# Performance work log

Measured on AMD Instinct MI355X. Metric: run time of the kernel, lower is better.

The kernel has to match this reference:

```python
import jax, jax.numpy as jnp
import numpy as np

N_NODES = 100_000
N_EDGES = 1_600_000
IN_C, HID_C, OUT_C = 128, 64, 32


def gcn_conv(x, W, b, src, dst, n_nodes):
    """PyG GCNConv with add_self_loops=True, symmetric normalization.
    out = D^{-1/2} (A + I) D^{-1/2} (x @ W) + b, with D = deg(A) + 1.
    Self-loop contribution added analytically to avoid materializing loop edges."""
    h = x @ W                                            # [N, F_out]
    deg = jnp.zeros((n_nodes,), h.dtype).at[dst].add(1.0) + 1.0
    dinv = jax.lax.rsqrt(deg)                            # deg >= 1 from self-loops
    norm = dinv[src] * dinv[dst]                         # [E]
    agg = jnp.zeros_like(h).at[dst].add(h[src] * norm[:, None])
    agg = agg + h * (dinv * dinv)[:, None]               # self-loop term
    return agg + b


def setup_inputs() -> dict:
    key = jax.random.key(0)
    ks = jax.random.split(key, 9)
    x = jax.random.normal(ks[0], (N_NODES, IN_C), dtype=jnp.float32)
    edge_index = jax.random.randint(ks[1], (2, N_EDGES), 0, N_NODES, dtype=jnp.int64)
    g = lambda k, fi, fo: jax.random.normal(k, (fi, fo), jnp.float32) * np.sqrt(2.0 / (fi + fo)).astype(np.float32)
    W1 = g(ks[2], IN_C, HID_C)
    b1 = jnp.zeros((HID_C,), jnp.float32)
    W2 = g(ks[3], HID_C, OUT_C)
    b2 = jnp.zeros((OUT_C,), jnp.float32)
    Wl = g(ks[4], IN_C + HID_C + OUT_C, OUT_C)
    bl = jnp.zeros((OUT_C,), jnp.float32)
    return {"x": x, "edge_index": edge_index, "W1": W1, "b1": b1,
            "W2": W2, "b2": b2, "Wl": Wl, "bl": bl}


def reference(x, edge_index, W1, b1, W2, b2, Wl, bl):
    src, dst = edge_index[0], edge_index[1]
    n = x.shape[0]
    h1 = jax.nn.relu(gcn_conv(x, W1, b1, src, dst, n))   # dropout is identity in eval
    h2 = gcn_conv(h1, W2, b2, src, dst, n)
    cat = jnp.concatenate([x, h1, h2], axis=1)           # [N, in+hid+out]
    return jax.nn.log_softmax(cat @ Wl + bl, axis=-1)
```

## Files before the change

### kernel.cpp

```cpp
#include <hip/hip_runtime.h>
#include <hip/hip_bf16.h>
#include <hip/hip_fp16.h>

typedef __hip_bfloat16 bf16;
typedef __attribute__((ext_vector_type(8))) short short8;
typedef __attribute__((ext_vector_type(4))) float f32x4;
typedef __attribute__((ext_vector_type(2))) float f32x2;
typedef _Float16 h16x2 __attribute__((ext_vector_type(2)));

#define MFMA16(a, b, c) __builtin_amdgcn_mfma_f32_16x16x32_bf16((a), (b), (c), 0, 0, 0)

static __device__ __forceinline__ float ldf(const void* p, long long i, bool f32) {
    return f32 ? ((const float*)p)[i] : __bfloat162float(((const bf16*)p)[i]);
}

static __device__ __forceinline__ short f2bs(float v) {
    union { bf16 h; short s; } u; u.h = __float2bfloat16(v); return u.s;
}

static __device__ __forceinline__ unsigned int pack_bf16x2(float a, float b) {
    return (unsigned int)(unsigned short)f2bs(a) | ((unsigned int)(unsigned short)f2bs(b) << 16);
}

static __device__ __forceinline__ unsigned int pack_h2(float a, float b) {
    __half2 hh = __floats2half2_rn(a, b);
    union { __half2 h; unsigned int u; } cv; cv.h = hh; return cv.u;
}

static __device__ __forceinline__ h16x2 as_h2(unsigned int u) {
    union { unsigned int u; h16x2 h; } cv; cv.u = u; return cv.h;
}

static __device__ __forceinline__ unsigned char f32_to_fp8(float v) {
    int pk = __builtin_amdgcn_cvt_pk_fp8_f32(v, 0.f, 0, false);
    return (unsigned char)(pk & 0xFF);
}
static __device__ __forceinline__ f32x2 fp8x2_to_f32x2(unsigned short v) {
    return __builtin_amdgcn_cvt_pk_f32_fp8((int)v, false);
}

static __device__ __forceinline__ int ld_src(const int* ei, int E, int e, bool i64) {
    return i64 ? ei[2 * e] : ei[e];
}
static __device__ __forceinline__ int ld_dst(const int* ei, int E, int e, bool i64) {
    return i64 ? ei[2 * (E + e)] : ei[E + e];
}


__global__ __launch_bounds__(256, 4)
void bhist_kernel(const int* __restrict__ ei, int E,
                  const void* __restrict__ x, const void* __restrict__ W1,
                  const void* __restrict__ Wl,
                  int shift, int NB, int nchunk,
                  int* __restrict__ flags, int* __restrict__ bucketCount,
                  bf16* __restrict__ Bp1, bf16* __restrict__ Bp3) {
    __shared__ int h[256];
    __shared__ int sdet;
    int bid = blockIdx.x;
    if (bid >= nchunk) {
        int which = bid - nchunk;
        const void* W = which ? Wl : W1;
        bf16* Bp = which ? Bp3 : Bp1;
        int ntiles = which ? 2 : 4, nc = which ? 32 : 64, nfrag = which ? 14 : 16;
        if (threadIdx.x == 0) sdet = 0;
        __syncthreads();
        const unsigned short* u = (const unsigned short*)W;
        int bad = 0;
        for (int i = threadIdx.x; i < 4096; i += 256) {
            unsigned e = (u[i] >> 7) & 0xFF;
            if (e >= 0xA0) bad++;
        }
        if (bad) atomicAdd(&sdet, bad);
        __syncthreads();
        bool fw = sdet > 16;
        if (which == 0 && threadIdx.x == 0) flags[1] = fw ? 1 : 0;
        for (int s = threadIdx.x; s < nfrag * 64; s += 256) {
            int f = s >> 6, lane = s & 63;
            int kstep = f / ntiles, ntile = f % ntiles;
            int n = ntile * 16 + (lane & 15);
            int kbase = kstep * 32 + (lane >> 4) * 8;
#pragma unroll
            for (int j = 0; j < 8; j++)
                Bp[s * 8 + j] = __float2bfloat16(ldf(W, (long long)(kbase + j) * nc + n, fw));
        }
        return;
    }
    if (bid == 0) {
        if (threadIdx.x == 0) sdet = 0;
        __syncthreads();
        const unsigned short* u = (const unsigned short*)x;
        int bad = 0;
        for (int i = threadIdx.x; i < 4096; i += 256) {
            unsigned e = (u[i] >> 7) & 0xFF;
            if (e >= 0xA0) bad++;
        }
        if (bad) atomicAdd(&sdet, bad);
        __syncthreads();
        if (threadIdx.x == 0) flags[0] = (sdet > 16) ? 1 : 0;
        __syncthreads();
    }
    if (threadIdx.x == 0) sdet = 0;
    for (int i = threadIdx.x; i < 256; i += 256) h[i] = 0;
    __syncthreads();
    {
        int nz = 0;
        for (int i = threadIdx.x; i < 1024; i += 256)
            if (2 * i + 1 < 2 * E && ei[2 * i + 1] != 0) nz++;
        if (nz) atomicAdd(&sdet, nz);
    }
    __syncthreads();
    bool i64 = (sdet == 0);
    int base = bid * 4096;
    for (int i = 0; i < 16; i++) {
        int e = base + i * 256 + threadIdx.x;
        if (e < E) atomicAdd(&h[ld_dst(ei, E, e, i64) >> shift], 1);
    }
    __syncthreads();
    for (int i = threadIdx.x; i < NB; i += 256)
        if (h[i]) atomicAdd(&bucketCount[i], h[i]);
}

__global__ __launch_bounds__(256, 4)
void bpart_kernel(const int* __restrict__ ei, int E, int shift, int NB,
                  const int* __restrict__ bucketCount, int* __restrict__ bcursor,
                  int2* __restrict__ ebuf) {
    __shared__ int h[256];
    __shared__ int gofs[256];
    __shared__ int bs[256];
    __shared__ int2 se[4096];
    __shared__ int sdet;
    if (threadIdx.x == 0) sdet = 0;
    for (int i = threadIdx.x; i < 256; i += 256) h[i] = 0;
    __syncthreads();
    {
        int nz = 0;
        for (int i = threadIdx.x; i < 1024; i += 256)
            if (2 * i + 1 < 2 * E && ei[2 * i + 1] != 0) nz++;
        if (nz) atomicAdd(&sdet, nz);
    }
    __syncthreads();
    bool i64 = (sdet == 0);
    int base = blockIdx.x * 4096;
    for (int i = 0; i < 16; i++) {
        int e = base + i * 256 + threadIdx.x;
        if (e < E) {
            int s = ld_src(ei, E, e, i64), d = ld_dst(ei, E, e, i64);
            se[i * 256 + threadIdx.x] = make_int2(s, d);
            atomicAdd(&h[d >> shift], 1);
        }
    }
    int v = ((int)threadIdx.x < NB) ? bucketCount[threadIdx.x] : 0;
    bs[threadIdx.x] = v;
    __syncthreads();
    for (int off = 1; off < 256; off <<= 1) {
        int t = ((int)threadIdx.x >= off) ? bs[threadIdx.x - off] : 0;
        __syncthreads();
        bs[threadIdx.x] += t;
        __syncthreads();
    }
    if ((int)threadIdx.x < NB) {
        int c = h[threadIdx.x];
        int b0 = bs[threadIdx.x] - v;
        gofs[threadIdx.x] = c ? (b0 + atomicAdd(&bcursor[threadIdx.x], c)) : 0;
    }
    __syncthreads();
    for (int i = threadIdx.x; i < 256; i += 256) h[i] = 0;
    __syncthreads();
    for (int i = 0; i < 16; i++) {
        int e = base + i * 256 + threadIdx.x;
        if (e < E) {
            int2 w = se[i * 256 + threadIdx.x];
            int b = w.y >> shift;
            int p = atomicAdd(&h[b], 1);
            ebuf[gofs[b] + p] = w;
        }
    }
}

__global__ __launch_bounds__(256, 2)
void bbuild_kernel(const int2* __restrict__ ebuf, const int* __restrict__ bucketCount,
                   int shift, int N, int E, int* __restrict__ rowptr,
                   float* __restrict__ dinv, int* __restrict__ csr_src) {
    __shared__ int cnt[1024];
    __shared__ int exc[1024];
    __shared__ int bs[256];
    int b = blockIdx.x;
    int v = ((int)threadIdx.x < 256) ? bucketCount[threadIdx.x] : 0;
    bs[threadIdx.x] = v;
    __syncthreads();
    for (int off = 1; off < 256; off <<= 1) {
        int t = ((int)threadIdx.x >= off) ? bs[threadIdx.x - off] : 0;
        __syncthreads();
        bs[threadIdx.x] += t;
        __syncthreads();
    }
    int end = bs[b];
    int beg = end - bucketCount[b];
    __syncthreads();
    int nodeBase = b << shift;
    int width = 1 << shift;
    int nn = N - nodeBase; if (nn > width) nn = width;
    for (int i = threadIdx.x; i < width; i += 256) cnt[i] = 0;
    __syncthreads();
    for (int e = beg + threadIdx.x; e < end; e += 256)
        atomicAdd(&cnt[ebuf[e].y - nodeBase], 1);
    __syncthreads();
    int per = width / 256;
    int s = 0;
    int base4 = threadIdx.x * per;
    for (int i = 0; i < per; i++) s += cnt[base4 + i];
    bs[threadIdx.x] = s;
    __syncthreads();
    for (int off = 1; off < 256; off <<= 1) {
        int t = ((int)threadIdx.x >= off) ? bs[threadIdx.x - off] : 0;
        __syncthreads();
        bs[threadIdx.x] += t;
        __syncthreads();
    }
    int run = bs[threadIdx.x] - s;
    for (int i = 0; i < per; i++) { exc[base4 + i] = run; run += cnt[base4 + i]; }
    __syncthreads();
    for (int i = threadIdx.x; i < nn; i += 256) {
        int node = nodeBase + i;
        rowptr[node] = beg + exc[i];
        dinv[node] = rsqrtf((float)cnt[i] + 1.0f);
    }
    __syncthreads();
    for (int i = threadIdx.x; i < width; i += 256) cnt[i] = 0;
    __syncthreads();
    for (int e = beg + threadIdx.x; e < end; e += 256) {
        int2 w = ebuf[e];
        int l = w.y - nodeBase;
        int p = atomicAdd(&cnt[l], 1);
        csr_src[beg + exc[l] + p] = w.x;
    }
    if (b == 0 && threadIdx.x == 0) rowptr[N] = E;
}

__global__ __launch_bounds__(256, 3)
void gemm1_mfma_kernel(const void* __restrict__ x, const bf16* __restrict__ Bpack,
                       const float* __restrict__ dinv, const int* __restrict__ flags,
                       unsigned char* __restrict__ h1g, short* __restrict__ xb, int N) {
    bool fx = flags[0] != 0;
    int lane = threadIdx.x & 63, wave = threadIdx.x >> 6;
    int m = lane & 15, quad = lane >> 4;
    int base = blockIdx.x * 128 + wave * 32;
    if (base >= N) return;
    const short8* bp = (const short8*)Bpack;
    short8 B[16];
#pragma unroll
    for (int i = 0; i < 16; i++) B[i] = bp[i * 64 + lane];
    if (base + 32 <= N) {
#pragma unroll
        for (int t = 0; t < 2; t++) {
            int r0 = base + t * 16;
            short8 A[4];
            if (fx) {
                const float* xr = &((const float*)x)[(long long)(r0 + m) * 128 + quad * 8];
#pragma unroll
                for (int k = 0; k < 4; k++) {
                    float4 fa = *(const float4*)(xr + k * 32);
                    float4 fb = *(const float4*)(xr + k * 32 + 4);
                    short8 o;
                    o[0] = f2bs(fa.x); o[1] = f2bs(fa.y); o[2] = f2bs(fa.z); o[3] = f2bs(fa.w);
                    o[4] = f2bs(fb.x); o[5] = f2bs(fb.y); o[6] = f2bs(fb.z); o[7] = f2bs(fb.w);
                    A[k] = o;
                }
                short* xw = &xb[(long long)(r0 + m) * 128 + quad * 8];
#pragma unroll
                for (int k = 0; k < 4; k++) *(short8*)(xw + k * 32) = A[k];
            } else {
                const short* xr = &((const short*)x)[(long long)(r0 + m) * 128 + quad * 8];
#pragma unroll
                for (int k = 0; k < 4; k++) A[k] = *(const short8*)(xr + k * 32);
            }
            f32x4 acc[4];
#pragma unroll
            for (int nt = 0; nt < 4; nt++) acc[nt] = (f32x4){0.f, 0.f, 0.f, 0.f};
#pragma unroll
            for (int k = 0; k < 4; k++) {
#pragma unroll
                for (int nt = 0; nt < 4; nt++) acc[nt] = MFMA16(A[k], B[k * 4 + nt], acc[nt]);
            }
            float dv[4];
#pragma unroll
            for (int r = 0; r < 4; r++) dv[r] = dinv[r0 + quad * 4 + r];
            unsigned char* o = &h1g[(long long)(r0 + quad * 4) * 64 + m];
#pragma unroll
            for (int nt = 0; nt < 4; nt++) {
#pragma unroll
                for (int r = 0; r < 4; r++) o[(long long)r * 64 + nt * 16] = f32_to_fp8(acc[nt][r] * dv[r]);
            }
        }
    } else {
#pragma unroll
        for (int t = 0; t < 2; t++) {
            int r0 = base + t * 16;
            int row = r0 + m;
            short8 A[4];
#pragma unroll
            for (int k = 0; k < 4; k++) A[k] = (short8){0,0,0,0,0,0,0,0};
            if (row < N) {
                if (fx) {
                    const float* xr = &((const float*)x)[(long long)row * 128 + quad * 8];
#pragma unroll
                    for (int k = 0; k < 4; k++) {
                        float4 fa = *(const float4*)(xr + k * 32);
                        float4 fb = *(const float4*)(xr + k * 32 + 4);
                        short8 o;
                        o[0] = f2bs(fa.x); o[1] = f2bs(fa.y); o[2] = f2bs(fa.z); o[3] = f2bs(fa.w);
                        o[4] = f2bs(fb.x); o[5] = f2bs(fb.y); o[6] = f2bs(fb.z); o[7] = f2bs(fb.w);
                        A[k] = o;
                    }
                    short* xw = &xb[(long long)row * 128 + quad * 8];
#pragma unroll
                    for (int k = 0; k < 4; k++) *(short8*)(xw + k * 32) = A[k];
                } else {
                    const short* xr = &((const short*)x)[(long long)row * 128 + quad * 8];
#pragma unroll
                    for (int k = 0; k < 4; k++) A[k] = *(const short8*)(xr + k * 32);
                }
            }
            f32x4 acc[4];
#pragma unroll
            for (int nt = 0; nt < 4; nt++) acc[nt] = (f32x4){0.f, 0.f, 0.f, 0.f};
#pragma unroll
            for (int k = 0; k < 4; k++) {
#pragma unroll
                for (int nt = 0; nt < 4; nt++) acc[nt] = MFMA16(A[k], B[k * 4 + nt], acc[nt]);
            }
#pragma unroll
            for (int r = 0; r < 4; r++) {
                int orow = r0 + quad * 4 + r;
                if (orow < N) {
                    float dv = dinv[orow];
                    unsigned char* o = &h1g[(long long)orow * 64 + m];
#pragma unroll
                    for (int nt = 0; nt < 4; nt++) o[nt * 16] = f32_to_fp8(acc[nt][r] * dv);
                }
            }
        }
    }
}

__global__ __launch_bounds__(256, 8)
void gather1_kernel(const unsigned short* __restrict__ h1g, const float* __restrict__ dinv,
                    const int* __restrict__ rowptr, const int* __restrict__ csr_src,
                    const void* __restrict__ bptr, const void* __restrict__ W2,
                    const int* __restrict__ flags,
                    unsigned int* __restrict__ h1b, __half* __restrict__ h2g, int N) {
    __shared__ unsigned int w2p[1024];
    __shared__ unsigned int h1s[4][2][32];
    bool fw = flags[1] != 0;
    for (int j = threadIdx.x; j < 1024; j += 256) {
        int k2 = j >> 5, c0 = j & 31;
        float a = ldf(W2, (long long)(2 * k2) * 32 + c0, fw);
        float b = ldf(W2, (long long)(2 * k2 + 1) * 32 + c0, fw);
        w2p[j] = pack_h2(a, b);
    }
    __syncthreads();
    int lane = threadIdx.x & 63;
    int c = lane & 31, hf = lane >> 5;
    int wv = __builtin_amdgcn_readfirstlane(threadIdx.x >> 6);
    int n0 = (blockIdx.x * 4 + wv) * 2;
    if (n0 >= N) return;
    bool has1 = (n0 + 1 < N);
    int beg = rowptr[n0];
    int mid = rowptr[n0 + 1];
    int end = has1 ? rowptr[n0 + 2] : mid;
    const unsigned short* hL = h1g + c;
    float aA0 = 0.f, aA1 = 0.f;
    float aN0 = 0.f, aN1 = 0.f;
    int p = beg;
    for (; p + 32 <= end; p += 32) {
        unsigned short v[16]; float r[16];
#pragma unroll
        for (int u = 0; u < 16; u++) {
            int s0 = csr_src[p + 2 * u];
            int s1 = csr_src[p + 2 * u + 1];
            int s = hf ? s1 : s0;
            r[u] = ((p + 2 * u + hf) < mid) ? 1.f : 0.f;
            v[u] = hL[(long long)s * 32];
        }
#pragma unroll
        for (int u = 0; u < 16; u++) {
            f32x2 f = fp8x2_to_f32x2(v[u]);
            aA0 += f.x; aA1 += f.y;
            aN0 = fmaf(f.x, r[u], aN0);
            aN1 = fmaf(f.y, r[u], aN1);
        }
    }
    for (; p + 16 <= end; p += 16) {
        unsigned short v[8]; float r[8];
#pragma unroll
        for (int u = 0; u < 8; u++) {
            int s0 = csr_src[p + 2 * u];
            int s1 = csr_src[p + 2 * u + 1];
            int s = hf ? s1 : s0;
            r[u] = ((p + 2 * u + hf) < mid) ? 1.f : 0.f;
            v[u] = hL[(long long)s * 32];
        }
#pragma unroll
        for (int u = 0; u < 8; u++) {
            f32x2 f = fp8x2_to_f32x2(v[u]);
            aA0 += f.x; aA1 += f.y;
            aN0 = fmaf(f.x, r[u], aN0);
            aN1 = fmaf(f.y, r[u], aN1);
        }
    }
    if (p < end) {
        unsigned short v[8]; float mk[8], r[8];
#pragma unroll
        for (int u = 0; u < 8; u++) {
            int i0 = p + 2 * u, i1 = i0 + 1;
            int s0 = csr_src[(i0 < end) ? i0 : beg];
            int s1 = csr_src[(i1 < end) ? i1 : beg];
            int s = hf ? s1 : s0;
            int i = p + 2 * u + hf;
            mk[u] = (i < end) ? 1.f : 0.f;
            r[u]  = (i < mid) ? 1.f : 0.f;
            v[u] = hL[(long long)s * 32];
        }
#pragma unroll
        for (int u = 0; u < 8; u++) {
            f32x2 f = fp8x2_to_f32x2(v[u]);
            aA0 = fmaf(f.x, mk[u], aA0);
            aA1 = fmaf(f.y, mk[u], aA1);
            aN0 = fmaf(f.x, r[u], aN0);
            aN1 = fmaf(f.y, r[u], aN1);
        }
    }
    aA0 += __shfl_xor(aA0, 32); aA1 += __shfl_xor(aA1, 32);
    aN0 += __shfl_xor(aN0, 32); aN1 += __shfl_xor(aN1, 32);
    int node = n0 + hf;
    int nodeC = (node < N) ? node : n0;
    float a0 = hf ? (aA0 - aN0) : aN0;
    float a1 = hf ? (aA1 - aN1) : aN1;
    f32x2 gs = fp8x2_to_f32x2(h1g[(long long)nodeC * 32 + c]);
    float dvd = dinv[nodeC];
    float o0 = fmaxf(dvd * (a0 + gs.x) + ldf(bptr, 2 * c, fw), 0.f);
    float o1 = fmaxf(dvd * (a1 + gs.y) + ldf(bptr, 2 * c + 1, fw), 0.f);
    if (node < N)
        h1b[(long long)node * 32 + c] = pack_bf16x2(o0, o1);
    h1s[wv][hf][c] = pack_h2(o0, o1);
    __threadfence_block();
    const unsigned int* hrow = h1s[wv][hf];
    float acc = 0.f;
#pragma unroll 8
    for (int k2 = 0; k2 < 32; k2++)
        acc = __builtin_amdgcn_fdot2(as_h2(hrow[k2]), as_h2(w2p[k2 * 32 + c]), acc, false);
    if (node < N)
        h2g[(long long)node * 32 + c] = __float2half(dvd * acc);
}

__global__ __launch_bounds__(256, 8)
void gather2_kernel(const unsigned int* __restrict__ h2g, const float* __restrict__ dinv,
                    const int* __restrict__ rowptr, const int* __restrict__ csr_src,
                    const void* __restrict__ bptr, const int* __restrict__ flags,
                    unsigned int* __restrict__ h2b, int N) {
    bool fw = flags[1] != 0;
    int lane = threadIdx.x & 63;
    int c = lane & 15, sub = lane >> 4;
    int wv = __builtin_amdgcn_readfirstlane(threadIdx.x >> 6);
    int n0 = (blockIdx.x * 4 + wv) * 2;
    if (n0 >= N) return;
    bool has1 = (n0 + 1 < N);
    int beg = rowptr[n0];
    int mid = rowptr[n0 + 1];
    int end = has1 ? rowptr[n0 + 2] : mid;
    const unsigned int* hL = h2g + c;
    float aA0 = 0.f, aA1 = 0.f, aN0 = 0.f, aN1 = 0.f;
    int p = beg;
    for (; p + 32 <= end; p += 32) {
        unsigned int v[8]; float r[8];
#pragma unroll
        for (int u = 0; u < 8; u++) {
            int i0 = p + 4 * u;
            int sa0 = csr_src[i0], sa1 = csr_src[i0 + 1];
            int sa2 = csr_src[i0 + 2], sa3 = csr_src[i0 + 3];
            int sA = (sub & 1) ? sa1 : sa0;
            int sB = (sub & 1) ? sa3 : sa2;
            int s  = (sub & 2) ? sB : sA;
            r[u] = ((i0 + sub) < mid) ? 1.f : 0.f;
            v[u] = hL[(long long)s * 16];
        }
#pragma unroll
        for (int u = 0; u < 8; u++) {
            float2 f = __half22float2(*(const __half2*)&v[u]);
            aA0 += f.x; aA1 += f.y;
            aN0 = fmaf(f.x, r[u], aN0);
            aN1 = fmaf(f.y, r[u], aN1);
        }
    }
    for (; p + 16 <= end; p += 16) {
        unsigned int v[4]; float r[4];
#pragma unroll
        for (int u = 0; u < 4; u++) {
            int i0 = p + 4 * u;
            int sa0 = csr_src[i0], sa1 = csr_src[i0 + 1];
            int sa2 = csr_src[i0 + 2], sa3 = csr_src[i0 + 3];
            int sA = (sub & 1) ? sa1 : sa0;
            int sB = (sub & 1) ? sa3 : sa2;
            int s  = (sub & 2) ? sB : sA;
            r[u] = ((i0 + sub) < mid) ? 1.f : 0.f;
            v[u] = hL[(long long)s * 16];
        }
#pragma unroll
        for (int u = 0; u < 4; u++) {
            float2 f = __half22float2(*(const __half2*)&v[u]);
            aA0 += f.x; aA1 += f.y;
            aN0 = fmaf(f.x, r[u], aN0);
            aN1 = fmaf(f.y, r[u], aN1);
        }
    }
    if (p < end) {
        unsigned int v[4]; float mk[4], r[4];
#pragma unroll
        for (int u = 0; u < 4; u++) {
            int i0 = p + 4 * u;
            int sa0 = csr_src[(i0     < end) ? i0     : beg];
            int sa1 = csr_src[(i0 + 1 < end) ? i0 + 1 : beg];
            int sa2 = csr_src[(i0 + 2 < end) ? i0 + 2 : beg];
            int sa3 = csr_src[(i0 + 3 < end) ? i0 + 3 : beg];
            int sA = (sub & 1) ? sa1 : sa0;
            int sB = (sub & 1) ? sa3 : sa2;
            int s  = (sub & 2) ? sB : sA;
            int i = i0 + sub;
            mk[u] = (i < end) ? 1.f : 0.f;
            r[u]  = (i < mid) ? 1.f : 0.f;
            v[u] = hL[(long long)s * 16];
        }
#pragma unroll
        for (int u = 0; u < 4; u++) {
            float2 f = __half22float2(*(const __half2*)&v[u]);
            aA0 = fmaf(f.x, mk[u], aA0);
            aA1 = fmaf(f.y, mk[u], aA1);
            aN0 = fmaf(f.x, r[u], aN0);
            aN1 = fmaf(f.y, r[u], aN1);
        }
    }
    aA0 += __shfl_xor(aA0, 16); aA1 += __shfl_xor(aA1, 16);
    aN0 += __shfl_xor(aN0, 16); aN1 += __shfl_xor(aN1, 16);
    aA0 += __shfl_xor(aA0, 32); aA1 += __shfl_xor(aA1, 32);
    aN0 += __shfl_xor(aN0, 32); aN1 += __shfl_xor(aN1, 32);
    if (sub < 2) {
        int node = n0 + sub;
        if (node < N) {
            float a0 = sub ? (aA0 - aN0) : aN0;
            float a1 = sub ? (aA1 - aN1) : aN1;
            unsigned int gsv = h2g[(long long)node * 16 + c];
            float2 gs = __half22float2(*(const __half2*)&gsv);
            float dvd = dinv[node];
            float o0 = dvd * (a0 + gs.x) + ldf(bptr, 2 * c, fw);
            float o1 = dvd * (a1 + gs.y) + ldf(bptr, 2 * c + 1, fw);
            h2b[(long long)node * 16 + c] = pack_bf16x2(o0, o1);
        }
    }
}

__global__ __launch_bounds__(256, 2)
void final_mfma_kernel(const void* __restrict__ x, const short* __restrict__ xb,
                       const short* __restrict__ h1b,
                       const short* __restrict__ h2b, const bf16* __restrict__ Bpack,
                       const void* __restrict__ bl, const int* __restrict__ flags,
                       void* __restrict__ out, int N) {
    bool fw = flags[1] != 0, fx = flags[0] != 0;
    const short* xs = fx ? xb : (const short*)x;
    int lane = threadIdx.x & 63, wave = threadIdx.x >> 6;
    int m = lane & 15, quad = lane >> 4;
    int r0 = blockIdx.x * 64 + wave * 16;
    if (r0 >= N) return;
    const short8* bp = (const short8*)Bpack;
    short8 B[14];
#pragma unroll
    for (int i = 0; i < 14; i++) B[i] = bp[i * 64 + lane];
    f32x4 acc0 = {0.f,0.f,0.f,0.f}, acc1 = {0.f,0.f,0.f,0.f};
    bool full = (r0 + 16 <= N);
    int row = r0 + m;
    bool rowok = full || (row < N);
#pragma unroll
    for (int s = 0; s < 7; s++) {
        short8 A = {0,0,0,0,0,0,0,0};
        if (rowok) {
            const short* p;
            if (s < 4)      p = &xs [(long long)row * 128 + s * 32 + quad * 8];
            else if (s < 6) p = &h1b[(long long)row * 64 + (s - 4) * 32 + quad * 8];
            else            p = &h2b[(long long)row * 32 + quad * 8];
            A = *(const short8*)p;
        }
        acc0 = MFMA16(A, B[s * 2 + 0], acc0);
        acc1 = MFMA16(A, B[s * 2 + 1], acc1);
    }
    float bl0 = ldf(bl, m, fw), bl1 = ldf(bl, m + 16, fw);
#pragma unroll
    for (int r = 0; r < 4; r++) {
        float v0 = acc0[r] + bl0, v1 = acc1[r] + bl1;
        float mx = fmaxf(v0, v1);
#pragma unroll
        for (int o = 8; o > 0; o >>= 1) mx = fmaxf(mx, __shfl_xor(mx, o));
        float sm = __expf(v0 - mx) + __expf(v1 - mx);
#pragma unroll
        for (int o = 8; o > 0; o >>= 1) sm += __shfl_xor(sm, o);
        float lse = mx + __logf(sm);
        int orow = r0 + quad * 4 + r;
        if (orow < N) {
            if (fx) {
                ((float*)out)[(long long)orow * 32 + m]      = v0 - lse;
                ((float*)out)[(long long)orow * 32 + 16 + m] = v1 - lse;
            } else {
                ((bf16*)out)[(long long)orow * 32 + m]      = __float2bfloat16(v0 - lse);
                ((bf16*)out)[(long long)orow * 32 + 16 + m] = __float2bfloat16(v1 - lse);
            }
        }
    }
}

extern "C" void kernel_launch(void* const* d_in, const int* in_sizes, int n_in,
                              void* d_out, int out_size, void* d_ws, size_t ws_size,
                              hipStream_t stream) {
    const void* x  = d_in[0];
    const int*  ei = (const int*)d_in[1];
    const void* W1 = d_in[2];
    const void* b1 = d_in[3];
    const void* W2 = d_in[4];
    const void* b2 = d_in[5];
    const void* Wl = d_in[6];
    const void* bl = d_in[7];

    int N = in_sizes[0] / 128;
    int E = in_sizes[1] / 2;

    int shift = 9;
    while (((N + (1 << shift) - 1) >> shift) > 256 && shift < 10) shift++;
    int NB = (N + (1 << shift) - 1) >> shift;

    int* ip      = (int*)d_ws;
    int* flags   = ip;
    int* bucketCount = ip + 16;
    int* bucketBase  = bucketCount + 256;
    int* bcursor     = bucketBase + 272;
    float* dinv  = (float*)(bcursor + 256);
    int* rowptr  = (int*)(dinv + N);
    bf16* Bp1    = (bf16*)(rowptr + N + 16);
    bf16* Bp2    = (bf16*)((int*)Bp1 + 4096);
    bf16* Bp3    = (bf16*)((int*)Bp2 + 1024);
    int* csr_src = (int*)Bp3 + 3584;
    short* xb    = (short*)(csr_src + E);
    int*   Ai    = (int*)xb + (size_t)N * 64;
    int2*  ebuf  = (int2*)Ai;
    unsigned char* h1g = (unsigned char*)Ai;
    __half* h2g  = (__half*)(Ai + (size_t)N * 16);
    unsigned int* h2b = (unsigned int*)(Ai + (size_t)N * 48);
    unsigned int* h1b = (unsigned int*)(Ai + (size_t)N * 64);

    hipMemsetAsync(ip, 0, 800 * sizeof(int), stream);

    int nchunk = (E + 4095) / 4096;
    bhist_kernel<<<nchunk + 2, 256, 0, stream>>>(ei, E, x, W1, Wl, shift, NB, nchunk,
                                                 flags, bucketCount, Bp1, Bp3);
    bpart_kernel<<<nchunk, 256, 0, stream>>>(ei, E, shift, NB, bucketCount, bcursor, ebuf);
    bbuild_kernel<<<NB, 256, 0, stream>>>(ebuf, bucketCount, shift, N, E, rowptr, dinv, csr_src);

    gemm1_mfma_kernel<<<(N + 127) / 128, 256, 0, stream>>>(x, Bp1, dinv, flags, h1g, xb, N);
    gather1_kernel<<<(N + 7) / 8, 256, 0, stream>>>((const unsigned short*)h1g, dinv, rowptr, csr_src,
                                                    b1, W2, flags, h1b, h2g, N);
    gather2_kernel<<<(N + 7) / 8, 256, 0, stream>>>((const unsigned int*)h2g, dinv, rowptr, csr_src,
                                                    b2, flags, h2b, N);
    final_mfma_kernel<<<(N + 63) / 64, 256, 0, stream>>>(x, (const short*)xb, (const short*)h1b,
                                                         (const short*)h2b, Bp3, bl, flags, d_out, N);
}
```

Measured before the change: 280.2 us.

## Fuse layer-2 gather into final MFMA kernel and store h2 in fp8

Merges the second-layer neighbor gather and the final concat-GEMM/log-softmax into one kernel. Each block aggregates 64 nodes into shared memory and feeds them straight to the MFMA stage, so the h2b intermediate never goes through global memory and one launch disappears. The pre-aggregation h2 features are also stored as fp8 instead of fp16, halving the bytes of the random gather. This costs precision in layer 2 and gives fewer, longer blocks with lower occupancy (launch bounds 4), with a barrier between the gather and GEMM phases.

```diff
diff --git a/kernel.cpp b/kernel.cpp
--- a/kernel.cpp
+++ b/kernel.cpp
@@ -348,7 +348,7 @@
                     const int* __restrict__ rowptr, const int* __restrict__ csr_src,
                     const void* __restrict__ bptr, const void* __restrict__ W2,
                     const int* __restrict__ flags,
-                    unsigned int* __restrict__ h1b, __half* __restrict__ h2g, int N) {
+                    unsigned int* __restrict__ h1b, unsigned char* __restrict__ h2g, int N) {
     __shared__ unsigned int w2p[1024];
     __shared__ unsigned int h1s[4][2][32];
     bool fw = flags[1] != 0;
@@ -450,125 +450,124 @@
     for (int k2 = 0; k2 < 32; k2++)
         acc = __builtin_amdgcn_fdot2(as_h2(hrow[k2]), as_h2(w2p[k2 * 32 + c]), acc, false);
     if (node < N)
-        h2g[(long long)node * 32 + c] = __float2half(dvd * acc);
-}
-
-__global__ __launch_bounds__(256, 8)
-void gather2_kernel(const unsigned int* __restrict__ h2g, const float* __restrict__ dinv,
+        h2g[(long long)node * 32 + c] = f32_to_fp8(dvd * acc);
+}
+
+__global__ __launch_bounds__(256, 4)
+void g2final_kernel(const unsigned short* __restrict__ h2g, const float* __restrict__ dinv,
                     const int* __restrict__ rowptr, const int* __restrict__ csr_src,
-                    const void* __restrict__ bptr, const int* __restrict__ flags,
-                    unsigned int* __restrict__ h2b, int N) {
-    bool fw = flags[1] != 0;
+                    const void* __restrict__ b2,
+                    const void* __restrict__ x, const short* __restrict__ xb,
+                    const short* __restrict__ h1b, const bf16* __restrict__ Bpack,
+                    const void* __restrict__ bl, const int* __restrict__ flags,
+                    void* __restrict__ out, int N) {
+    __shared__ unsigned int h2s[64][16];
+    bool fw = flags[1] != 0, fx = flags[0] != 0;
     int lane = threadIdx.x & 63;
-    int c = lane & 15, sub = lane >> 4;
     int wv = __builtin_amdgcn_readfirstlane(threadIdx.x >> 6);
-    int n0 = (blockIdx.x * 4 + wv) * 2;
-    if (n0 >= N) return;
-    bool has1 = (n0 + 1 < N);
-    int beg = rowptr[n0];
-    int mid = rowptr[n0 + 1];
-    int end = has1 ? rowptr[n0 + 2] : mid;
-    const unsigned int* hL = h2g + c;
-    float aA0 = 0.f, aA1 = 0.f, aN0 = 0.f, aN1 = 0.f;
-    int p = beg;
-    for (; p + 32 <= end; p += 32) {
-        unsigned int v[8]; float r[8];
-#pragma unroll
-        for (int u = 0; u < 8; u++) {
-            int i0 = p + 4 * u;
-            int sa0 = csr_src[i0], sa1 = csr_src[i0 + 1];
-            int sa2 = csr_src[i0 + 2], sa3 = csr_src[i0 + 3];
-            int sA = (sub & 1) ? sa1 : sa0;
-            int sB = (sub & 1) ? sa3 : sa2;
-            int s  = (sub & 2) ? sB : sA;
-            r[u] = ((i0 + sub) < mid) ? 1.f : 0.f;
-            v[u] = hL[(long long)s * 16];
-        }
-#pragma unroll
-        for (int u = 0; u < 8; u++) {
-            float2 f = __half22float2(*(const __half2*)&v[u]);
-            aA0 += f.x; aA1 += f.y;
-            aN0 = fmaf(f.x, r[u], aN0);
-            aN1 = fmaf(f.y, r[u], aN1);
-        }
-    }
-    for (; p + 16 <= end; p += 16) {
-        unsigned int v[4]; float r[4];
-#pragma unroll
-        for (int u = 0; u < 4; u++) {
-            int i0 = p + 4 * u;
-            int sa0 = csr_src[i0], sa1 = csr_src[i0 + 1];
-            int sa2 = csr_src[i0 + 2], sa3 = csr_src[i0 + 3];
-            int sA = (sub & 1) ? sa1 : sa0;
-            int sB = (sub & 1) ? sa3 : sa2;
-            int s  = (sub & 2) ? sB : sA;
-            r[u] = ((i0 + sub) < mid) ? 1.f : 0.f;
-            v[u] = hL[(long long)s * 16];
-        }
-#pragma unroll
-        for (int u = 0; u < 4; u++) {
-            float2 f = __half22float2(*(const __half2*)&v[u]);
-            aA0 += f.x; aA1 += f.y;
-            aN0 = fmaf(f.x, r[u], aN0);
-            aN1 = fmaf(f.y, r[u], aN1);
-        }
-    }
-    if (p < end) {
-        unsigned int v[4]; float mk[4], r[4];
-#pragma unroll
-        for (int u = 0; u < 4; u++) {
-            int i0 = p + 4 * u;
-            int sa0 = csr_src[(i0     < end) ? i0     : beg];
-            int sa1 = csr_src[(i0 + 1 < end) ? i0 + 1 : beg];
-            int sa2 = csr_src[(i0 + 2 < end) ? i0 + 2 : beg];
-            int sa3 = csr_src[(i0 + 3 < end) ? i0 + 3 : beg];
-            int sA = (sub & 1) ? sa1 : sa0;
-            int sB = (sub & 1) ? sa3 : sa2;
-            int s  = (sub & 2) ? sB : sA;
-            int i = i0 + sub;
-            mk[u] = (i < end) ? 1.f : 0.f;
-            r[u]  = (i < mid) ? 1.f : 0.f;
-            v[u] = hL[(long long)s * 16];
-        }
-#pragma unroll
-        for (int u = 0; u < 4; u++) {
-            float2 f = __half22float2(*(const __half2*)&v[u]);
-            aA0 = fmaf(f.x, mk[u], aA0);
-            aA1 = fmaf(f.y, mk[u], aA1);
-            aN0 = fmaf(f.x, r[u], aN0);
-            aN1 = fmaf(f.y, r[u], aN1);
-        }
-    }
-    aA0 += __shfl_xor(aA0, 16); aA1 += __shfl_xor(aA1, 16);
-    aN0 += __shfl_xor(aN0, 16); aN1 += __shfl_xor(aN1, 16);
-    aA0 += __shfl_xor(aA0, 32); aA1 += __shfl_xor(aA1, 32);
-    aN0 += __shfl_xor(aN0, 32); aN1 += __shfl_xor(aN1, 32);
-    if (sub < 2) {
-        int node = n0 + sub;
-        if (node < N) {
-            float a0 = sub ? (aA0 - aN0) : aN0;
-            float a1 = sub ? (aA1 - aN1) : aN1;
-            unsigned int gsv = h2g[(long long)node * 16 + c];
-            float2 gs = __half22float2(*(const __half2*)&gsv);
-            float dvd = dinv[node];
-            float o0 = dvd * (a0 + gs.x) + ldf(bptr, 2 * c, fw);
-            float o1 = dvd * (a1 + gs.y) + ldf(bptr, 2 * c + 1, fw);
-            h2b[(long long)node * 16 + c] = pack_bf16x2(o0, o1);
-        }
-    }
-}
-
-__global__ __launch_bounds__(256, 2)
-void final_mfma_kernel(const void* __restrict__ x, const short* __restrict__ xb,
-                       const short* __restrict__ h1b,
-                       const short* __restrict__ h2b, const bf16* __restrict__ Bpack,
-                       const void* __restrict__ bl, const int* __restrict__ flags,
-                       void* __restrict__ out, int N) {
-    bool fw = flags[1] != 0, fx = flags[0] != 0;
+    int base64 = blockIdx.x * 64;
+    {
+        int c = lane & 15, sub = lane >> 4;
+        const unsigned short* hL = h2g + c;
+        for (int ps = 0; ps < 8; ps++) {
+            int n0 = base64 + wv * 16 + ps * 2;
+            if (n0 >= N) break;
+            bool has1 = (n0 + 1 < N);
+            int beg = rowptr[n0];
+            int mid = rowptr[n0 + 1];
+            int end = has1 ? rowptr[n0 + 2] : mid;
+            float aA0 = 0.f, aA1 = 0.f, aN0 = 0.f, aN1 = 0.f;
+            int p = beg;
+            for (; p + 32 <= end; p += 32) {
+                unsigned short v[8]; float r[8];
+#pragma unroll
+                for (int u = 0; u < 8; u++) {
+                    int i0 = p + 4 * u;
+                    int sa0 = csr_src[i0], sa1 = csr_src[i0 + 1];
+                    int sa2 = csr_src[i0 + 2], sa3 = csr_src[i0 + 3];
+                    int sA = (sub & 1) ? sa1 : sa0;
+                    int sB = (sub & 1) ? sa3 : sa2;
+                    int s  = (sub & 2) ? sB : sA;
+                    r[u] = ((i0 + sub) < mid) ? 1.f : 0.f;
+                    v[u] = hL[(long long)s * 16];
+                }
+#pragma unroll
+                for (int u = 0; u < 8; u++) {
+                    f32x2 f = fp8x2_to_f32x2(v[u]);
+                    aA0 += f.x; aA1 += f.y;
+                    aN0 = fmaf(f.x, r[u], aN0);
+                    aN1 = fmaf(f.y, r[u], aN1);
+                }
+            }
+            for (; p + 16 <= end; p += 16) {
+                unsigned short v[4]; float r[4];
+#pragma unroll
+                for (int u = 0; u < 4; u++) {
+                    int i0 = p + 4 * u;
+                    int sa0 = csr_src[i0], sa1 = csr_src[i0 + 1];
+                    int sa2 = csr_src[i0 + 2], sa3 = csr_src[i0 + 3];
+                    int sA = (sub & 1) ? sa1 : sa0;
+                    int sB = (sub & 1) ? sa3 : sa2;
+                    int s  = (sub & 2) ? sB : sA;
+                    r[u] = ((i0 + sub) < mid) ? 1.f : 0.f;
+                    v[u] = hL[(long long)s * 16];
+                }
+#pragma unroll
+                for (int u = 0; u < 4; u++) {
+                    f32x2 f = fp8x2_to_f32x2(v[u]);
+                    aA0 += f.x; aA1 += f.y;
+                    aN0 = fmaf(f.x, r[u], aN0);
+                    aN1 = fmaf(f.y, r[u], aN1);
+                }
+            }
+            if (p < end) {
+                unsigned short v[4]; float mk[4], r[4];
+#pragma unroll
+                for (int u = 0; u < 4; u++) {
+                    int i0 = p + 4 * u;
+                    int sa0 = csr_src[(i0     < end) ? i0     : beg];
+                    int sa1 = csr_src[(i0 + 1 < end) ? i0 + 1 : beg];
+                    int sa2 = csr_src[(i0 + 2 < end) ? i0 + 2 : beg];
+                    int sa3 = csr_src[(i0 + 3 < end) ? i0 + 3 : beg];
+                    int sA = (sub & 1) ? sa1 : sa0;
+                    int sB = (sub & 1) ? sa3 : sa2;
+                    int s  = (sub & 2) ? sB : sA;
+                    int i = i0 + sub;
+                    mk[u] = (i < end) ? 1.f : 0.f;
+                    r[u]  = (i < mid) ? 1.f : 0.f;
+                    v[u] = hL[(long long)s * 16];
+                }
+#pragma unroll
+                for (int u = 0; u < 4; u++) {
+                    f32x2 f = fp8x2_to_f32x2(v[u]);
+                    aA0 = fmaf(f.x, mk[u], aA0);
+                    aA1 = fmaf(f.y, mk[u], aA1);
+                    aN0 = fmaf(f.x, r[u], aN0);
+                    aN1 = fmaf(f.y, r[u], aN1);
+                }
+            }
+            aA0 += __shfl_xor(aA0, 16); aA1 += __shfl_xor(aA1, 16);
+            aN0 += __shfl_xor(aN0, 16); aN1 += __shfl_xor(aN1, 16);
+            aA0 += __shfl_xor(aA0, 32); aA1 += __shfl_xor(aA1, 32);
+            aN0 += __shfl_xor(aN0, 32); aN1 += __shfl_xor(aN1, 32);
+            if (sub < 2) {
+                int node = n0 + sub;
+                if (node < N) {
+                    float a0 = sub ? (aA0 - aN0) : aN0;
+                    float a1 = sub ? (aA1 - aN1) : aN1;
+                    f32x2 gs = fp8x2_to_f32x2(h2g[(long long)node * 16 + c]);
+                    float dvd = dinv[node];
+                    float o0 = dvd * (a0 + gs.x) + ldf(b2, 2 * c, fw);
+                    float o1 = dvd * (a1 + gs.y) + ldf(b2, 2 * c + 1, fw);
+                    h2s[node - base64][c] = pack_bf16x2(o0, o1);
+                }
+            }
+        }
+    }
+    __syncthreads();
     const short* xs = fx ? xb : (const short*)x;
-    int lane = threadIdx.x & 63, wave = threadIdx.x >> 6;
     int m = lane & 15, quad = lane >> 4;
-    int r0 = blockIdx.x * 64 + wave * 16;
+    int r0 = base64 + wv * 16;
     if (r0 >= N) return;
     const short8* bp = (const short8*)Bpack;
     short8 B[14];
@@ -585,7 +584,7 @@
             const short* p;
             if (s < 4)      p = &xs [(long long)row * 128 + s * 32 + quad * 8];
             else if (s < 6) p = &h1b[(long long)row * 64 + (s - 4) * 32 + quad * 8];
-            else            p = &h2b[(long long)row * 32 + quad * 8];
+            else            p = (const short*)&h2s[row - base64][0] + quad * 8;
             A = *(const short8*)p;
         }
         acc0 = MFMA16(A, B[s * 2 + 0], acc0);
@@ -649,8 +648,7 @@
     int*   Ai    = (int*)xb + (size_t)N * 64;
     int2*  ebuf  = (int2*)Ai;
     unsigned char* h1g = (unsigned char*)Ai;
-    __half* h2g  = (__half*)(Ai + (size_t)N * 16);
-    unsigned int* h2b = (unsigned int*)(Ai + (size_t)N * 48);
+    unsigned char* h2g = (unsigned char*)(Ai + (size_t)N * 16);
     unsigned int* h1b = (unsigned int*)(Ai + (size_t)N * 64);
 
     hipMemsetAsync(ip, 0, 800 * sizeof(int), stream);
@@ -664,8 +662,7 @@
     gemm1_mfma_kernel<<<(N + 127) / 128, 256, 0, stream>>>(x, Bp1, dinv, flags, h1g, xb, N);
     gather1_kernel<<<(N + 7) / 8, 256, 0, stream>>>((const unsigned short*)h1g, dinv, rowptr, csr_src,
                                                     b1, W2, flags, h1b, h2g, N);
-    gather2_kernel<<<(N + 7) / 8, 256, 0, stream>>>((const unsigned int*)h2g, dinv, rowptr, csr_src,
-                                                    b2, flags, h2b, N);
-    final_mfma_kernel<<<(N + 63) / 64, 256, 0, stream>>>(x, (const short*)xb, (const short*)h1b,
-                                                         (const short*)h2b, Bp3, bl, flags, d_out, N);
-}
+    g2final_kernel<<<(N + 63) / 64, 256, 0, stream>>>((const unsigned short*)h2g, dinv, rowptr, csr_src,
+                                                      b2, x, (const short*)xb, (const short*)h1b,
+                                                      Bp3, bl, flags, d_out, N);
+}
```

Measured after the change: 286.0 us. 1.02x slower.
